# Kernel tuning notes

Hardware: AMD Instinct MI355X
Metric: run time of the kernel (lower is better)

## Reference

```python
import jax, jax.numpy as jnp
import numpy as np

RO = 4.0
STRIDE = 1.0
DILATIONS = (1, 1, 1, 2, 2, 4, 4)  # deep-snake res blocks


def conv2d(x, w, b, pad):
    y = jax.lax.conv_general_dilated(x, w, (1, 1), [(pad, pad), (pad, pad)],
                                     dimension_numbers=('NCHW', 'OIHW', 'NCHW'))
    return y + b[None, :, None, None]


def circ_conv(x, w, b, dilation):
    # x: [N, C, V]; circular (wrap) padding of n_adj*dilation on each side, kernel size 9 (n_adj=4)
    pad = (w.shape[-1] // 2) * dilation
    xp = jnp.concatenate([x[..., -pad:], x, x[..., :pad]], axis=-1)
    y = jax.lax.conv_general_dilated(xp, w, (1,), 'VALID', rhs_dilation=(dilation,),
                                     dimension_numbers=('NCH', 'OIH', 'NCH'))
    return y + b[None, :, None]


def bn(x, gamma, beta):
    # BatchNorm1d in eval mode (running_mean=0, running_var=1)
    return x * gamma[None, :, None] + beta[None, :, None]


def conv1x1(x, w, b):
    return jnp.einsum('oc,ncv->nov', w, x) + b[None, :, None]


def grid_sample_polys(feat, polys, ind):
    # feat: [B, C, H, W]; polys: [N, V, 2] (x, y) in feature-map pixel coords; ind: [N]
    # torch grid_sample(bilinear, align_corners=False, zeros pad) after the deep-snake
    # normalization x/(w/2)-1 reduces to sampling at (px-0.5, py-0.5).
    B, C, H, W = feat.shape
    ix = polys[..., 0] - 0.5
    iy = polys[..., 1] - 0.5
    x0 = jnp.floor(ix)
    y0 = jnp.floor(iy)
    wx = (ix - x0)[..., None]
    wy = (iy - y0)[..., None]
    x0i = x0.astype(jnp.int32)
    y0i = y0.astype(jnp.int32)

    def gather(yi, xi):
        valid = (xi >= 0) & (xi < W) & (yi >= 0) & (yi < H)
        xc = jnp.clip(xi, 0, W - 1)
        yc = jnp.clip(yi, 0, H - 1)
        v = feat[ind[:, None], :, yc, xc]  # [N, V, C]
        return v * valid[..., None]

    v00 = gather(y0i, x0i)
    v01 = gather(y0i, x0i + 1)
    v10 = gather(y0i + 1, x0i)
    v11 = gather(y0i + 1, x0i + 1)
    out = (v00 * (1 - wx) * (1 - wy) + v01 * wx * (1 - wy)
           + v10 * (1 - wx) * wy + v11 * wx * wy)
    return out.transpose(0, 2, 1)  # [N, C, V]


def snake_forward(x, head_w, head_b, head_g, head_bt, res_w, res_b, res_g, res_bt,
                  fus_w, fus_b, pw1, pb1, pw2, pb2, pw3, pb3):
    # Deep-snake Snake with conv_type='dgrid': head + 7 residual dilated circular convs,
    # fusion 1x1 + global max pool, then 3-layer 1x1 prediction head -> 2 offsets.
    h = bn(jax.nn.relu(circ_conv(x, head_w, head_b, 1)), head_g, head_bt)
    states = [h]
    cur = h
    for i, d in enumerate(DILATIONS):
        y = bn(jax.nn.relu(circ_conv(cur, res_w[i], res_b[i], d)), res_g[i], res_bt[i])
        cur = y + cur
        states.append(cur)
    state = jnp.concatenate(states, axis=1)  # [N, 8*state_dim, V]
    g = conv1x1(state, fus_w, fus_b)
    g = jnp.max(g, axis=2, keepdims=True)
    g = jnp.broadcast_to(g, (state.shape[0], g.shape[1], state.shape[2]))
    s = jnp.concatenate([g, state], axis=1)
    h1 = jax.nn.relu(conv1x1(s, pw1, pb1))
    h2 = jax.nn.relu(conv1x1(h1, pw2, pb2))
    return conv1x1(h2, pw3, pb3)  # [N, 2, V]


def setup_inputs() -> dict:
    key = jax.random.key(0)
    ks = jax.random.split(key, 24)
    B, C_IN, H, W = 8, 66, 128, 128
    NP, V = 128, 128
    SD = 128           # Snake state_dim = num_vertex
    FD = 66            # snake feature_dim = c_out_proj + 2
    K = 9              # 2*n_adj + 1
    nres = len(DILATIONS)
    s = 0.01  # torch init: normal_(0, 0.01)
    inp = {
        'cnn_feature': jax.random.normal(ks[0], (B, C_IN, H, W), jnp.float32),
        'i_it_poly': jax.random.uniform(ks[1], (NP, V, 2), jnp.float32) * (W - 1),
        'c_it_poly': jax.random.normal(ks[2], (NP, V, 2), jnp.float32) * 0.25,
        'ind': jax.random.randint(ks[3], (NP,), 0, B, jnp.int32),
        'proj_w1': jax.random.normal(ks[4], (256, C_IN, 3, 3), jnp.float32) * s,
        'proj_b1': jnp.zeros((256,), jnp.float32),
        'proj_w2': jax.random.normal(ks[5], (64, 256, 1, 1), jnp.float32) * s,
        'proj_b2': jnp.zeros((64,), jnp.float32),
        'head_w': jax.random.normal(ks[6], (SD, FD, K), jnp.float32) * s,
        'head_b': jnp.zeros((SD,), jnp.float32),
        'head_g': jnp.ones((SD,), jnp.float32),
        'head_bt': jnp.zeros((SD,), jnp.float32),
        'res_w': jax.random.normal(ks[7], (nres, SD, SD, K), jnp.float32) * s,
        'res_b': jnp.zeros((nres, SD), jnp.float32),
        'res_g': jnp.ones((nres, SD), jnp.float32),
        'res_bt': jnp.zeros((nres, SD), jnp.float32),
        'fus_w': jax.random.normal(ks[8], (256, SD * (nres + 1)), jnp.float32) * s,
        'fus_b': jnp.zeros((256,), jnp.float32),
        'pw1': jax.random.normal(ks[9], (256, SD * (nres + 1) + 256), jnp.float32) * s,
        'pb1': jnp.zeros((256,), jnp.float32),
        'pw2': jax.random.normal(ks[10], (64, 256), jnp.float32) * s,
        'pb2': jnp.zeros((64,), jnp.float32),
        'pw3': jax.random.normal(ks[11], (2, 64), jnp.float32) * s,
        'pb3': jnp.zeros((2,), jnp.float32),
    }
    return inp


def reference(cnn_feature, i_it_poly, c_it_poly, ind,
              proj_w1, proj_b1, proj_w2, proj_b2,
              head_w, head_b, head_g, head_bt,
              res_w, res_b, res_g, res_bt,
              fus_w, fus_b, pw1, pb1, pw2, pb2, pw3, pb3):
    # projection: conv3x3 -> relu -> conv1x1  (66 -> 256 -> 64)
    feat = jax.nn.relu(conv2d(cnn_feature, proj_w1, proj_b1, 1))
    feat = conv2d(feat, proj_w2, proj_b2, 0)
    # gather per-vertex features via bilinear grid sampling (get_gcn_feature)
    vert_feat = grid_sample_polys(feat, i_it_poly, ind)          # [N, 64, V]
    coords = (c_it_poly * RO).transpose(0, 2, 1)                  # [N, 2, V]
    init_input = jnp.concatenate([vert_feat, coords], axis=1)     # [N, 66, V]
    offset = snake_forward(init_input, head_w, head_b, head_g, head_bt,
                           res_w, res_b, res_g, res_bt,
                           fus_w, fus_b, pw1, pb1, pw2, pb2, pw3, pb3)
    i_poly = i_it_poly * RO + offset.transpose(0, 2, 1) * STRIDE  # [N, V, 2]
    return i_poly
```

## Files before the change

### kernel.cpp

```cpp
#include <hip/hip_runtime.h>
#include <hip/hip_bf16.h>

constexpr int B   = 8;
constexpr int CIN = 66;
constexpr int H   = 128, W = 128;
constexpr int C1  = 256;
constexpr int NP  = 128;
constexpr int V   = 128;
constexpr int SD  = 128;
constexpr int NRES = 7;
constexpr float RO = 4.0f;

typedef __bf16 bf16x8 __attribute__((ext_vector_type(8)));
typedef float  f32x4  __attribute__((ext_vector_type(4)));
typedef unsigned short u16x8 __attribute__((ext_vector_type(8)));

__device__ inline float bfu2f(unsigned short u) {
    union { unsigned int i; float f; } c; c.i = ((unsigned)u) << 16; return c.f;
}

__global__ __launch_bounds__(256) void k_pack_x(const float* __restrict__ x,
                                                __hip_bfloat16* __restrict__ xp)
{
    const int bi  = blockIdx.x;
    const int b   = bi / 130;
    const int yp  = bi % 130;
    const int tid = threadIdx.x;
    const int y   = yp - 1;
    const bool interior = (y >= 0 && y < H);

    __shared__ float xs[CIN * W];
    if (interior) {
        for (int i = tid; i < CIN * W; i += 256)
            xs[i] = x[((size_t)b * CIN + (i >> 7)) * (H * W) + y * W + (i & 127)];
    }
    __syncthreads();
    __hip_bfloat16* op = xp + ((size_t)b * 130 + yp) * (130 * 72);
    for (int i = tid; i < 130 * 72; i += 256) {
        int xpx = i / 72, c = i - xpx * 72;
        int xx = xpx - 1;
        float v = 0.f;
        if (interior && xx >= 0 && xx < W && c < CIN) v = xs[c * W + xx];
        op[i] = __float2bfloat16(v);
    }
}

__global__ __launch_bounds__(256) void k_pack_weights(
    const float* __restrict__ w3, const float* __restrict__ hw,
    const float* __restrict__ rw, const float* __restrict__ fw,
    const float* __restrict__ ppw1, const float* __restrict__ ppw2,
    __hip_bfloat16* __restrict__ wp2, __hip_bfloat16* __restrict__ wpk2,
    __hip_bfloat16* __restrict__ fwb, __hip_bfloat16* __restrict__ pw1hb,
    __hip_bfloat16* __restrict__ pw2b)
{
    const int bid = blockIdx.x, tid = threadIdx.x;
    if (bid < 256) {
        int oc = bid;
        for (int t = tid; t < 3 * 232; t += 256) {
            int ky = t / 232, s = t - ky * 232;
            float v = 0.f;
            if (s < 216) {
                int kx = s / 72, ic = s - kx * 72;
                if (ic < CIN) v = w3[((size_t)(oc * CIN + ic) * 3 + ky) * 3 + kx];
            }
            wp2[((size_t)ky * 256 + oc) * 232 + s] = __float2bfloat16(v);
        }
    } else if (bid < 1280) {
        int q = bid - 256, l = q >> 7, oc = q & 127;
        for (int t = tid; t < 9 * 128; t += 256) {
            int k = t >> 7, ic = t & 127;
            float v = 0.f;
            if (l == 0) { if (ic < 66) v = hw[((size_t)oc * 66 + ic) * 9 + k]; }
            else v = rw[((((size_t)(l - 1) * 128 + oc) * 128) + ic) * 9 + k];
            int s = ic >> 3, j = ic & 7;
            int sw = ((s ^ (oc & 7)) << 3) + j;
            wpk2[(((size_t)l * 9 + k) * 128 + oc) * 128 + sw] = __float2bfloat16(v);
        }
    } else if (bid < 1536) {
        int r = bid - 1280;
        for (int c = tid; c < 1024; c += 256)
            fwb[(size_t)r * 1024 + c] = __float2bfloat16(fw[(size_t)r * 1024 + c]);
    } else if (bid < 1792) {
        int r = bid - 1536;
        for (int c = tid; c < 1024; c += 256)
            pw1hb[(size_t)r * 1024 + c] = __float2bfloat16(ppw1[(size_t)r * 1280 + 256 + c]);
    } else {
        int r = bid - 1792;
        for (int c = tid; c < 256; c += 256)
            pw2b[(size_t)r * 256 + c] = __float2bfloat16(ppw2[(size_t)r * 256 + c]);
    }
}

__global__ __launch_bounds__(256, 2) void k_conv3x3_mfma(
    const __hip_bfloat16* __restrict__ xp,
    const __hip_bfloat16* __restrict__ wp,
    const float* __restrict__ bias,
    __hip_bfloat16* __restrict__ out)
{
    constexpr int SB = 232;
    __shared__ __hip_bfloat16 ash[9392];
    __shared__ __hip_bfloat16 bsh[128 * SB];

    const int tid = threadIdx.x;
    const int ln  = tid & 63;
    const int wv  = tid >> 6;
    const int wm  = (wv >> 1) * 64;
    const int wn  = (wv & 1) * 64;
    const int l15 = ln & 15;
    const int lhi = ln >> 4;

    const int by  = blockIdx.x;
    const int b   = by >> 7;
    const int y   = by & 127;
    const int ocb = blockIdx.y * 128;

    if (tid < 32) ash[9360 + tid] = __float2bfloat16(0.f);

    f32x4 acc[4][4] = {};

    for (int ky = 0; ky < 3; ++ky) {
        __syncthreads();
        {
            const char* g = (const char*)(xp + ((size_t)b * 130 + y + ky) * 9360);
            for (int off = wv * 1024; off < 18720; off += 4096) {
                int o = off + ln * 16;
                if (o < 18720)
                    __builtin_amdgcn_global_load_lds(
                        (const __attribute__((address_space(1))) void*)(g + o),
                        (__attribute__((address_space(3))) void*)((char*)ash + off),
                        16, 0, 0);
            }
        }
        {
            const char* g = (const char*)(wp + ((size_t)ky * 256 + ocb) * SB);
            for (int off = wv * 1024; off < 59392; off += 4096) {
                int o = off + ln * 16;
                if (o < 59392)
                    __builtin_amdgcn_global_load_lds(
                        (const __attribute__((address_space(1))) void*)(g + o),
                        (__attribute__((address_space(3))) void*)((char*)bsh + off),
                        16, 0, 0);
            }
        }
        __syncthreads();

#pragma unroll
        for (int ks = 0; ks < 7; ++ks) {
            bf16x8 a[4], bq[4];
#pragma unroll
            for (int m = 0; m < 4; ++m) {
                int pos = wm + m * 16 + l15;
                a[m] = *(const bf16x8*)((const char*)ash + pos * 144 + ks * 64 + lhi * 16);
            }
#pragma unroll
            for (int n = 0; n < 4; ++n) {
                int oc = wn + n * 16 + l15;
                bq[n] = *(const bf16x8*)((const char*)bsh + oc * (SB * 2) + ks * 64 + lhi * 16);
            }
#pragma unroll
            for (int m = 0; m < 4; ++m)
#pragma unroll
                for (int n = 0; n < 4; ++n)
                    acc[m][n] = __builtin_amdgcn_mfma_f32_16x16x32_bf16(
                        a[m], bq[n], acc[m][n], 0, 0, 0);
        }
    }

#pragma unroll
    for (int n = 0; n < 4; ++n) {
        int oc = ocb + wn + n * 16 + l15;
        float bb = bias[oc];
#pragma unroll
        for (int m = 0; m < 4; ++m) {
#pragma unroll
            for (int r = 0; r < 4; ++r) {
                int pos = wm + m * 16 + lhi * 4 + r;
                float v = acc[m][n][r] + bb;
                v = v > 0.f ? v : 0.f;
                out[(((size_t)b * 128 + y) * 128 + pos) * 256 + oc] = __float2bfloat16(v);
            }
        }
    }
}

__global__ __launch_bounds__(256) void k_conv1x1_mfma(
    const __hip_bfloat16* __restrict__ feat1,
    const __hip_bfloat16* __restrict__ w2b,
    const float* __restrict__ b2,
    __hip_bfloat16* __restrict__ feat2)
{
    const int tid = threadIdx.x;
    const int ln  = tid & 63;
    const int wv  = tid >> 6;
    const int wm  = wv * 64;
    const int l15 = ln & 15;
    const int lhi = ln >> 4;
    const int pos0 = blockIdx.x * 256;

    __shared__ __hip_bfloat16 wsh[64 * 136];
    for (int i = tid; i < 1024; i += 256) {
        int row = i >> 4, slot = i & 15;
        *(bf16x8*)&wsh[row * 136 + slot * 8] = *(const bf16x8*)(w2b + row * 256 + slot * 8);
    }
    __syncthreads();

    f32x4 acc[4][4] = {};
#pragma unroll
    for (int kk = 0; kk < 8; ++kk) {
        bf16x8 a[4], bq[4];
#pragma unroll
        for (int m = 0; m < 4; ++m)
            a[m] = *(const bf16x8*)(feat1 + (size_t)(pos0 + wm + m * 16 + l15) * 256 + kk * 32 + lhi * 8);
#pragma unroll
        for (int n = 0; n < 4; ++n)
            bq[n] = *(const bf16x8*)&wsh[(n * 16 + l15) * 136 + kk * 32 + lhi * 8];
#pragma unroll
        for (int m = 0; m < 4; ++m)
#pragma unroll
            for (int n = 0; n < 4; ++n)
                acc[m][n] = __builtin_amdgcn_mfma_f32_16x16x32_bf16(a[m], bq[n], acc[m][n], 0, 0, 0);
    }
#pragma unroll
    for (int n = 0; n < 4; ++n) {
        int og = n * 16 + l15;
        float bb = b2[og];
#pragma unroll
        for (int m = 0; m < 4; ++m)
#pragma unroll
            for (int r = 0; r < 4; ++r) {
                int pos = pos0 + wm + m * 16 + lhi * 4 + r;
                feat2[(size_t)pos * 64 + og] = __float2bfloat16(acc[m][n][r] + bb);
            }
    }
}

__global__ __launch_bounds__(256) void k_sample(
    const __hip_bfloat16* __restrict__ feat2, const float* __restrict__ ipoly,
    const float* __restrict__ cpoly, const int* __restrict__ ind,
    __hip_bfloat16* __restrict__ X0)
{
    const int p = blockIdx.x;
    const int v = threadIdx.x & 127;
    const int half = threadIdx.x >> 7;

    float px = ipoly[(p * V + v) * 2 + 0];
    float py = ipoly[(p * V + v) * 2 + 1];
    float ix = px - 0.5f, iy = py - 0.5f;
    float x0f = floorf(ix), y0f = floorf(iy);
    float wx = ix - x0f, wy = iy - y0f;
    int x0 = (int)x0f, y0 = (int)y0f;

    int   xsv[2] = {x0, x0 + 1}, ysv[2] = {y0, y0 + 1};
    float wxs[2] = {1.f - wx, wx}, wys[2] = {1.f - wy, wy};
    float cw[4]; int cbase[4];
#pragma unroll
    for (int jy = 0; jy < 2; ++jy)
#pragma unroll
        for (int jx = 0; jx < 2; ++jx) {
            int xi = xsv[jx], yi = ysv[jy];
            bool ok = (xi >= 0) && (xi < W) && (yi >= 0) && (yi < H);
            int xc = min(max(xi, 0), W - 1);
            int yc = min(max(yi, 0), H - 1);
            cw[jy * 2 + jx]    = wys[jy] * wxs[jx] * (ok ? 1.f : 0.f);
            cbase[jy * 2 + jx] = yc * W + xc;
        }

    const __hip_bfloat16* fb = feat2 + (size_t)ind[p] * (16384 * 64);
    __hip_bfloat16* xr = X0 + ((size_t)p * V + v) * 128;
#pragma unroll
    for (int ch = 0; ch < 4; ++ch) {
        int chh = half * 4 + ch;
        float s[8];
#pragma unroll
        for (int e = 0; e < 8; ++e) s[e] = 0.f;
#pragma unroll
        for (int j = 0; j < 4; ++j) {
            u16x8 t = *(const u16x8*)(fb + (size_t)cbase[j] * 64 + chh * 8);
#pragma unroll
            for (int e = 0; e < 8; ++e) s[e] += cw[j] * bfu2f(t[e]);
        }
#pragma unroll
        for (int e = 0; e < 8; ++e) xr[chh * 8 + e] = __float2bfloat16(s[e]);
    }
    if (half) {
        xr[64] = __float2bfloat16(cpoly[(p * V + v) * 2 + 0] * RO);
        xr[65] = __float2bfloat16(cpoly[(p * V + v) * 2 + 1] * RO);
        for (int c = 66; c < 128; ++c) xr[c] = __float2bfloat16(0.f);
    }
}

__global__ __launch_bounds__(256) void k_snake_mfma(
    const __hip_bfloat16* __restrict__ xin,
    const __hip_bfloat16* __restrict__ wl,
    const float* __restrict__ bias, const float* __restrict__ gamma,
    const float* __restrict__ beta,
    const __hip_bfloat16* __restrict__ resin,
    __hip_bfloat16* __restrict__ out,
    int dil)
{
    const int tid = threadIdx.x;
    const int ln  = tid & 63;
    const int wv  = tid >> 6;
    const int wm  = (wv >> 1) * 64;
    const int wn  = (wv & 1) * 32;
    const int l15 = ln & 15;
    const int lhi = ln >> 4;
    const int p   = blockIdx.x;
    const int ocb = blockIdx.y * 64;

    __shared__ __hip_bfloat16 xs[128 * 136];
    __shared__ __hip_bfloat16 wsh[2 * 64 * 128];

    {
        const char* g = (const char*)(wl + (size_t)ocb * 128);
        for (int off = tid * 16; off < 16384; off += 4096)
            __builtin_amdgcn_global_load_lds(
                (const __attribute__((address_space(1))) void*)(g + off),
                (__attribute__((address_space(3))) void*)((char*)wsh + off), 16, 0, 0);
    }
    const __hip_bfloat16* xb = xin + (size_t)p * (V * 128);
    for (int i = tid; i < 2048; i += 256) {
        int r = i >> 4, slot = i & 15;
        *(bf16x8*)&xs[r * 136 + slot * 8] = *(const bf16x8*)(xb + r * 128 + slot * 8);
    }
    __syncthreads();

    f32x4 acc[4][2] = {};
#pragma unroll 1
    for (int k = 0; k < 9; ++k) {
        if (k < 8) {
            const char* g = (const char*)(wl + (size_t)(k + 1) * (128 * 128) + (size_t)ocb * 128);
            char* dst = (char*)wsh + ((k + 1) & 1) * 16384;
            for (int off = tid * 16; off < 16384; off += 4096)
                __builtin_amdgcn_global_load_lds(
                    (const __attribute__((address_space(1))) void*)(g + off),
                    (__attribute__((address_space(3))) void*)(dst + off), 16, 0, 0);
        }
        const __hip_bfloat16* wbuf = wsh + (k & 1) * 8192;
        const int ofs = (k - 4) * dil + 256;
#pragma unroll
        for (int kc = 0; kc < 4; ++kc) {
            bf16x8 a[4], bq[2];
#pragma unroll
            for (int m = 0; m < 4; ++m) {
                int row = (wm + m * 16 + l15 + ofs) & 127;
                a[m] = *(const bf16x8*)&xs[row * 136 + kc * 32 + lhi * 8];
            }
#pragma unroll
            for (int n = 0; n < 2; ++n) {
                int row  = wn + n * 16 + l15;
                int slot = (kc * 4 + lhi) ^ (row & 7);
                bq[n] = *(const bf16x8*)&wbuf[row * 128 + slot * 8];
            }
#pragma unroll
            for (int m = 0; m < 4; ++m)
#pragma unroll
                for (int n = 0; n < 2; ++n)
                    acc[m][n] = __builtin_amdgcn_mfma_f32_16x16x32_bf16(a[m], bq[n], acc[m][n], 0, 0, 0);
        }
        __syncthreads();
    }

#pragma unroll
    for (int n = 0; n < 2; ++n) {
        int oc = ocb + wn + n * 16 + l15;
        float bb = bias[oc], gg = gamma[oc], bt = beta[oc];
#pragma unroll
        for (int m = 0; m < 4; ++m)
#pragma unroll
            for (int r = 0; r < 4; ++r) {
                int pos = wm + m * 16 + lhi * 4 + r;
                size_t idx = ((size_t)p * V + pos) * 128 + oc;
                float v = acc[m][n][r] + bb;
                v = v > 0.f ? v : 0.f;
                v = v * gg + bt;
                if (resin) v += __bfloat162float(resin[idx]);
                out[idx] = __float2bfloat16(v);
            }
    }
}

__global__ __launch_bounds__(256) void k_vconv1024(
    const __hip_bfloat16* __restrict__ xin,
    const __hip_bfloat16* __restrict__ wb,
    const float* __restrict__ fbias,
    const float* __restrict__ pbias,
    int relu,
    __hip_bfloat16* __restrict__ out)
{
    const int tid = threadIdx.x;
    const int ln  = tid & 63;
    const int wv  = tid >> 6;
    const int wm  = (wv >> 1) * 64;
    const int wn  = (wv & 1) * 64;
    const int l15 = ln & 15;
    const int lhi = ln >> 4;
    const int p   = blockIdx.x;
    const int ocb = blockIdx.y * 128;

    f32x4 acc[4][4] = {};
    for (int s = 0; s < 8; ++s) {
        const __hip_bfloat16* xa = xin + ((size_t)s * NP + p) * (V * 128);
#pragma unroll
        for (int kc = 0; kc < 4; ++kc) {
            bf16x8 a[4], bq[4];
#pragma unroll
            for (int m = 0; m < 4; ++m)
                a[m] = *(const bf16x8*)(xa + (size_t)(wm + m * 16 + l15) * 128 + kc * 32 + lhi * 8);
#pragma unroll
            for (int n = 0; n < 4; ++n)
                bq[n] = *(const bf16x8*)(wb + (size_t)(ocb + wn + n * 16 + l15) * 1024 + s * 128 + kc * 32 + lhi * 8);
#pragma unroll
            for (int m = 0; m < 4; ++m)
#pragma unroll
                for (int n = 0; n < 4; ++n)
                    acc[m][n] = __builtin_amdgcn_mfma_f32_16x16x32_bf16(a[m], bq[n], acc[m][n], 0, 0, 0);
        }
    }
#pragma unroll
    for (int n = 0; n < 4; ++n) {
        int og = ocb + wn + n * 16 + l15;
        float bb = (fbias ? fbias[og] : 0.f) + (pbias ? pbias[(size_t)p * 256 + og] : 0.f);
#pragma unroll
        for (int m = 0; m < 4; ++m)
#pragma unroll
            for (int r = 0; r < 4; ++r) {
                int pos = wm + m * 16 + lhi * 4 + r;
                float v = acc[m][n][r] + bb;
                if (relu) v = v > 0.f ? v : 0.f;
                out[((size_t)p * V + pos) * 256 + og] = __float2bfloat16(v);
            }
    }
}

__global__ __launch_bounds__(128) void k_h2(
    const __hip_bfloat16* __restrict__ h1,
    const __hip_bfloat16* __restrict__ w2b,
    const float* __restrict__ pb2,
    __hip_bfloat16* __restrict__ h2)
{
    const int tid = threadIdx.x;
    const int ln  = tid & 63;
    const int wv  = tid >> 6;
    const int wm  = wv * 64;
    const int l15 = ln & 15;
    const int lhi = ln >> 4;
    const int p   = blockIdx.x;

    f32x4 acc[4][4] = {};
#pragma unroll
    for (int kk = 0; kk < 8; ++kk) {
        bf16x8 a[4], bq[4];
#pragma unroll
        for (int m = 0; m < 4; ++m)
            a[m] = *(const bf16x8*)(h1 + ((size_t)p * V + wm + m * 16 + l15) * 256 + kk * 32 + lhi * 8);
#pragma unroll
        for (int n = 0; n < 4; ++n)
            bq[n] = *(const bf16x8*)(w2b + (size_t)(n * 16 + l15) * 256 + kk * 32 + lhi * 8);
#pragma unroll
        for (int m = 0; m < 4; ++m)
#pragma unroll
            for (int n = 0; n < 4; ++n)
                acc[m][n] = __builtin_amdgcn_mfma_f32_16x16x32_bf16(a[m], bq[n], acc[m][n], 0, 0, 0);
    }
#pragma unroll
    for (int n = 0; n < 4; ++n) {
        int og = n * 16 + l15;
        float bb = pb2[og];
#pragma unroll
        for (int m = 0; m < 4; ++m)
#pragma unroll
            for (int r = 0; r < 4; ++r) {
                int pos = wm + m * 16 + lhi * 4 + r;
                float v = acc[m][n][r] + bb;
                v = v > 0.f ? v : 0.f;
                h2[((size_t)p * V + pos) * 64 + og] = __float2bfloat16(v);
            }
    }
}

__global__ __launch_bounds__(256) void k_gmaxgc(const __hip_bfloat16* __restrict__ fused,
                                                const float* __restrict__ pw1,
                                                const float* __restrict__ pb1,
                                                float* __restrict__ gc)
{
    int p = blockIdx.x, o = threadIdx.x;
    float m = -3.4e38f;
    for (int v = 0; v < V; ++v)
        m = fmaxf(m, __bfloat162float(fused[((size_t)p * V + v) * 256 + o]));
    __shared__ float gl[256];
    gl[o] = m;
    __syncthreads();
    float a = pb1[o];
    const float* wr = pw1 + (size_t)o * 1280;
    for (int c = 0; c < 256; ++c) a += wr[c] * gl[c];
    gc[(size_t)p * 256 + o] = a;
}

__global__ __launch_bounds__(128) void k_final(const __hip_bfloat16* __restrict__ h2,
                                               const float* __restrict__ pw3,
                                               const float* __restrict__ pb3,
                                               const float* __restrict__ ipoly,
                                               float* __restrict__ outp)
{
    int p = blockIdx.x, v = threadIdx.x;
    __shared__ float w3[128];
    w3[v] = pw3[v];
    __syncthreads();
    float a0 = pb3[0], a1 = pb3[1];
    const u16x8* hp = (const u16x8*)(h2 + ((size_t)p * V + v) * 64);
#pragma unroll
    for (int ch = 0; ch < 8; ++ch) {
        u16x8 t = hp[ch];
#pragma unroll
        for (int e = 0; e < 8; ++e) {
            int c = ch * 8 + e;
            float hv = bfu2f(t[e]);
            a0 += w3[c] * hv;
            a1 += w3[64 + c] * hv;
        }
    }
    int idx = (p * V + v) * 2;
    outp[idx]     = ipoly[idx] * RO + a0;
    outp[idx + 1] = ipoly[idx + 1] * RO + a1;
}

extern "C" void kernel_launch(void* const* d_in, const int* in_sizes, int n_in,
                              void* d_out, int out_size, void* d_ws, size_t ws_size,
                              hipStream_t stream)
{
    const float* cnn   = (const float*)d_in[0];
    const float* ipoly = (const float*)d_in[1];
    const float* cpoly = (const float*)d_in[2];
    const int*   ind   = (const int*)d_in[3];
    const float* pw1c  = (const float*)d_in[4];
    const float* pb1c  = (const float*)d_in[5];
    const float* pw2c  = (const float*)d_in[6];
    const float* pb2c  = (const float*)d_in[7];
    const float* hw    = (const float*)d_in[8];
    const float* hb    = (const float*)d_in[9];
    const float* hg    = (const float*)d_in[10];
    const float* hbt   = (const float*)d_in[11];
    const float* rw    = (const float*)d_in[12];
    const float* rb    = (const float*)d_in[13];
    const float* rg    = (const float*)d_in[14];
    const float* rbt   = (const float*)d_in[15];
    const float* fw    = (const float*)d_in[16];
    const float* fb    = (const float*)d_in[17];
    const float* ppw1  = (const float*)d_in[18];
    const float* ppb1  = (const float*)d_in[19];
    const float* ppw2  = (const float*)d_in[20];
    const float* ppb2  = (const float*)d_in[21];
    const float* ppw3  = (const float*)d_in[22];
    const float* ppb3  = (const float*)d_in[23];
    float* outp = (float*)d_out;

    char* ws = (char*)d_ws;
    __hip_bfloat16* feat1  = (__hip_bfloat16*)(ws);
    __hip_bfloat16* states = (__hip_bfloat16*)(ws);
    __hip_bfloat16* fused  = (__hip_bfloat16*)(ws + 33554432);
    __hip_bfloat16* h1     = (__hip_bfloat16*)(ws + 41943040);
    __hip_bfloat16* h2     = (__hip_bfloat16*)(ws + 50331648);
    float*          gcbuf  = (float*)(ws + 52428800);
    __hip_bfloat16* xp     = (__hip_bfloat16*)(ws + 67108864);
    __hip_bfloat16* feat2  = (__hip_bfloat16*)(ws + 67108864);
    __hip_bfloat16* wp2    = (__hip_bfloat16*)(ws + 86577664);
    __hip_bfloat16* wpk2   = (__hip_bfloat16*)(ws + 86934016);
    __hip_bfloat16* fwb    = (__hip_bfloat16*)(ws + 89293312);
    __hip_bfloat16* pw1hb  = (__hip_bfloat16*)(ws + 89817600);
    __hip_bfloat16* pw2b   = (__hip_bfloat16*)(ws + 90341888);
    __hip_bfloat16* X0     = (__hip_bfloat16*)(ws + 90374656);

    k_pack_x<<<dim3(8 * 130), 256, 0, stream>>>(cnn, xp);
    k_pack_weights<<<dim3(1856), 256, 0, stream>>>(pw1c, hw, rw, fw, ppw1, ppw2,
                                                   wp2, wpk2, fwb, pw1hb, pw2b);

    k_conv3x3_mfma<<<dim3(1024, 2), 256, 0, stream>>>(xp, wp2, pb1c, feat1);
    k_conv1x1_mfma<<<dim3(512), 256, 0, stream>>>(feat1, pw2b, pb2c, feat2);
    k_sample<<<dim3(NP), 256, 0, stream>>>(feat2, ipoly, cpoly, ind, X0);

    k_snake_mfma<<<dim3(NP, 2), 256, 0, stream>>>(X0, wpk2, hb, hg, hbt, nullptr,
                                                  states, 1);
    const int dil[NRES] = {1, 1, 1, 2, 2, 4, 4};
    const size_t SSZ = (size_t)NP * V * 128;
    for (int i = 0; i < NRES; ++i) {
        const __hip_bfloat16* xin = states + (size_t)i * SSZ;
        __hip_bfloat16* yout      = states + (size_t)(i + 1) * SSZ;
        const __hip_bfloat16* wi  = wpk2 + (size_t)(i + 1) * 9 * 128 * 128;
        k_snake_mfma<<<dim3(NP, 2), 256, 0, stream>>>(xin, wi, rb + i * SD, rg + i * SD,
                                                      rbt + i * SD, xin, yout, dil[i]);
    }

    k_vconv1024<<<dim3(NP, 2), 256, 0, stream>>>(states, fwb, fb, nullptr, 0, fused);
    k_gmaxgc<<<dim3(NP), 256, 0, stream>>>(fused, ppw1, ppb1, gcbuf);
    k_vconv1024<<<dim3(NP, 2), 256, 0, stream>>>(states, pw1hb, nullptr, gcbuf, 1, h1);
    k_h2<<<dim3(NP), 128, 0, stream>>>(h1, pw2b, ppb2, h2);
    k_final<<<dim3(NP), 128, 0, stream>>>(h2, ppw3, ppb3, ipoly, outp);
}
```

Measured before the change: 453.1 us.

## Fuse snake layers, fusion conv and prediction head into one per-polygon kernel

Replaces the 8 snake-layer launches, the two 1024-channel vertex convs, the global-max kernel and the two prediction-head kernels with a single kernel. Each block owns one polygon and keeps the layer state ping-ponged in LDS. The fusion and first prediction-layer GEMMs are accumulated in registers layer by layer, so the per-layer states, fused and h1 buffers never travel through global memory. Weights are now read straight from global memory without LDS staging or swizzle, and only 128 blocks run, each with a large register accumulator footprint. That trades launch and global-memory overhead for lower parallelism and possible register spills.

```diff
diff --git a/kernel.cpp b/kernel.cpp
--- a/kernel.cpp
+++ b/kernel.cpp
@@ -18,6 +18,7 @@
 __device__ inline float bfu2f(unsigned short u) {
     union { unsigned int i; float f; } c; c.i = ((unsigned)u) << 16; return c.f;
 }
+__device__ inline float b2f(__hip_bfloat16 b) { return __bfloat162float(b); }
 
 __global__ __launch_bounds__(256) void k_pack_x(const float* __restrict__ x,
                                                 __hip_bfloat16* __restrict__ xp)
@@ -51,7 +52,7 @@
     const float* __restrict__ ppw1, const float* __restrict__ ppw2,
     __hip_bfloat16* __restrict__ wp2, __hip_bfloat16* __restrict__ wpk2,
     __hip_bfloat16* __restrict__ fwb, __hip_bfloat16* __restrict__ pw1hb,
-    __hip_bfloat16* __restrict__ pw2b)
+    __hip_bfloat16* __restrict__ pw2b, __hip_bfloat16* __restrict__ pw1gb)
 {
     const int bid = blockIdx.x, tid = threadIdx.x;
     if (bid < 256) {
@@ -72,9 +73,7 @@
             float v = 0.f;
             if (l == 0) { if (ic < 66) v = hw[((size_t)oc * 66 + ic) * 9 + k]; }
             else v = rw[((((size_t)(l - 1) * 128 + oc) * 128) + ic) * 9 + k];
-            int s = ic >> 3, j = ic & 7;
-            int sw = ((s ^ (oc & 7)) << 3) + j;
-            wpk2[(((size_t)l * 9 + k) * 128 + oc) * 128 + sw] = __float2bfloat16(v);
+            wpk2[(((size_t)l * 9 + k) * 128 + oc) * 128 + ic] = __float2bfloat16(v);
         }
     } else if (bid < 1536) {
         int r = bid - 1280;
@@ -84,10 +83,14 @@
         int r = bid - 1536;
         for (int c = tid; c < 1024; c += 256)
             pw1hb[(size_t)r * 1024 + c] = __float2bfloat16(ppw1[(size_t)r * 1280 + 256 + c]);
-    } else {
+    } else if (bid < 1856) {
         int r = bid - 1792;
         for (int c = tid; c < 256; c += 256)
             pw2b[(size_t)r * 256 + c] = __float2bfloat16(ppw2[(size_t)r * 256 + c]);
+    } else {
+        int o = bid - 1856;
+        for (int c = tid; c < 256; c += 256)
+            pw1gb[(size_t)c * 256 + o] = __float2bfloat16(ppw1[(size_t)o * 1280 + c]);
     }
 }
 
@@ -289,240 +292,222 @@
     }
 }
 
-__global__ __launch_bounds__(256) void k_snake_mfma(
-    const __hip_bfloat16* __restrict__ xin,
-    const __hip_bfloat16* __restrict__ wl,
-    const float* __restrict__ bias, const float* __restrict__ gamma,
-    const float* __restrict__ beta,
-    const __hip_bfloat16* __restrict__ resin,
-    __hip_bfloat16* __restrict__ out,
-    int dil)
-{
+__global__ __launch_bounds__(256, 1) void k_mega(
+    const __hip_bfloat16* __restrict__ X0,
+    const __hip_bfloat16* __restrict__ wsnk,
+    const float* __restrict__ hb, const float* __restrict__ hg, const float* __restrict__ hbt,
+    const float* __restrict__ rb, const float* __restrict__ rg, const float* __restrict__ rbt,
+    const __hip_bfloat16* __restrict__ fwb,
+    const float* __restrict__ fb,
+    const __hip_bfloat16* __restrict__ pw1gb,
+    const float* __restrict__ pb1,
+    const __hip_bfloat16* __restrict__ pw1hb,
+    const __hip_bfloat16* __restrict__ pw2b,
+    const float* __restrict__ pb2,
+    const float* __restrict__ pw3, const float* __restrict__ pb3,
+    const float* __restrict__ ipoly,
+    float* __restrict__ outp)
+{
+    __shared__ __hip_bfloat16 s0[128 * 136];
+    __shared__ __hip_bfloat16 s1[128 * 136];
+    __shared__ __hip_bfloat16 h1L[128 * 264];
+    __shared__ float gred[2048];
+    __shared__ float gl[256];
+    __shared__ float gcv[256];
+
     const int tid = threadIdx.x;
     const int ln  = tid & 63;
     const int wv  = tid >> 6;
-    const int wm  = (wv >> 1) * 64;
-    const int wn  = (wv & 1) * 32;
     const int l15 = ln & 15;
     const int lhi = ln >> 4;
+    const int wmv = (wv >> 1) * 64;
+    const int wns = (wv & 1) * 64;
+    const int wno = (wv & 1) * 128;
     const int p   = blockIdx.x;
-    const int ocb = blockIdx.y * 64;
-
-    __shared__ __hip_bfloat16 xs[128 * 136];
-    __shared__ __hip_bfloat16 wsh[2 * 64 * 128];
 
     {
-        const char* g = (const char*)(wl + (size_t)ocb * 128);
-        for (int off = tid * 16; off < 16384; off += 4096)
-            __builtin_amdgcn_global_load_lds(
-                (const __attribute__((address_space(1))) void*)(g + off),
-                (__attribute__((address_space(3))) void*)((char*)wsh + off), 16, 0, 0);
-    }
-    const __hip_bfloat16* xb = xin + (size_t)p * (V * 128);
-    for (int i = tid; i < 2048; i += 256) {
-        int r = i >> 4, slot = i & 15;
-        *(bf16x8*)&xs[r * 136 + slot * 8] = *(const bf16x8*)(xb + r * 128 + slot * 8);
-    }
-    __syncthreads();
-
-    f32x4 acc[4][2] = {};
+        const __hip_bfloat16* xb = X0 + (size_t)p * (V * 128);
+        for (int i = tid; i < 2048; i += 256) {
+            int r = i >> 4, slot = i & 15;
+            *(bf16x8*)&s0[r * 136 + slot * 8] = *(const bf16x8*)(xb + r * 128 + slot * 8);
+        }
+    }
+    __syncthreads();
+
+    f32x4 facc[4][8] = {};
+    f32x4 hacc[4][8] = {};
+    const int dils[8] = {1, 1, 1, 1, 2, 2, 4, 4};
+
 #pragma unroll 1
-    for (int k = 0; k < 9; ++k) {
-        if (k < 8) {
-            const char* g = (const char*)(wl + (size_t)(k + 1) * (128 * 128) + (size_t)ocb * 128);
-            char* dst = (char*)wsh + ((k + 1) & 1) * 16384;
-            for (int off = tid * 16; off < 16384; off += 4096)
-                __builtin_amdgcn_global_load_lds(
-                    (const __attribute__((address_space(1))) void*)(g + off),
-                    (__attribute__((address_space(3))) void*)(dst + off), 16, 0, 0);
-        }
-        const __hip_bfloat16* wbuf = wsh + (k & 1) * 8192;
-        const int ofs = (k - 4) * dil + 256;
+    for (int l = 0; l < 8; ++l) {
+        __hip_bfloat16* cur  = (l & 1) ? s1 : s0;
+        __hip_bfloat16* pong = (l & 1) ? s0 : s1;
+        const __hip_bfloat16* wl = wsnk + (size_t)l * (9 * 128 * 128);
+        const int dil = dils[l];
+
+        f32x4 sacc[4][4] = {};
+#pragma unroll 1
+        for (int k = 0; k < 9; ++k) {
+            const int ofs = (k - 4) * dil + 128;
+            const __hip_bfloat16* wk = wl + (size_t)k * (128 * 128);
+#pragma unroll
+            for (int kc = 0; kc < 4; ++kc) {
+                bf16x8 a[4], bq[4];
+#pragma unroll
+                for (int m = 0; m < 4; ++m) {
+                    int row = (wmv + m * 16 + l15 + ofs) & 127;
+                    a[m] = *(const bf16x8*)&cur[row * 136 + kc * 32 + lhi * 8];
+                }
+#pragma unroll
+                for (int n = 0; n < 4; ++n)
+                    bq[n] = *(const bf16x8*)(wk + (size_t)(wns + n * 16 + l15) * 128 + kc * 32 + lhi * 8);
+#pragma unroll
+                for (int m = 0; m < 4; ++m)
+#pragma unroll
+                    for (int n = 0; n < 4; ++n)
+                        sacc[m][n] = __builtin_amdgcn_mfma_f32_16x16x32_bf16(a[m], bq[n], sacc[m][n], 0, 0, 0);
+            }
+        }
+
+        const float* bbp = l ? (rb  + (l - 1) * 128) : hb;
+        const float* ggp = l ? (rg  + (l - 1) * 128) : hg;
+        const float* btp = l ? (rbt + (l - 1) * 128) : hbt;
+#pragma unroll
+        for (int n = 0; n < 4; ++n) {
+            int oc = wns + n * 16 + l15;
+            float bb = bbp[oc], gg = ggp[oc], bt = btp[oc];
+#pragma unroll
+            for (int m = 0; m < 4; ++m)
+#pragma unroll
+                for (int r = 0; r < 4; ++r) {
+                    int pos = wmv + m * 16 + lhi * 4 + r;
+                    float v = sacc[m][n][r] + bb;
+                    v = v > 0.f ? v : 0.f;
+                    v = v * gg + bt;
+                    if (l) v += b2f(cur[pos * 136 + oc]);
+                    pong[pos * 136 + oc] = __float2bfloat16(v);
+                }
+        }
+        __syncthreads();
+
 #pragma unroll
         for (int kc = 0; kc < 4; ++kc) {
-            bf16x8 a[4], bq[2];
-#pragma unroll
-            for (int m = 0; m < 4; ++m) {
-                int row = (wm + m * 16 + l15 + ofs) & 127;
-                a[m] = *(const bf16x8*)&xs[row * 136 + kc * 32 + lhi * 8];
-            }
-#pragma unroll
-            for (int n = 0; n < 2; ++n) {
-                int row  = wn + n * 16 + l15;
-                int slot = (kc * 4 + lhi) ^ (row & 7);
-                bq[n] = *(const bf16x8*)&wbuf[row * 128 + slot * 8];
-            }
+            bf16x8 a2[4], bqf[8], bqh[8];
+#pragma unroll
+            for (int m = 0; m < 4; ++m)
+                a2[m] = *(const bf16x8*)&pong[(wmv + m * 16 + l15) * 136 + kc * 32 + lhi * 8];
+#pragma unroll
+            for (int n = 0; n < 8; ++n) {
+                size_t row = (size_t)(wno + n * 16 + l15);
+                bqf[n] = *(const bf16x8*)(fwb   + row * 1024 + l * 128 + kc * 32 + lhi * 8);
+                bqh[n] = *(const bf16x8*)(pw1hb + row * 1024 + l * 128 + kc * 32 + lhi * 8);
+            }
+#pragma unroll
+            for (int m = 0; m < 4; ++m)
+#pragma unroll
+                for (int n = 0; n < 8; ++n) {
+                    facc[m][n] = __builtin_amdgcn_mfma_f32_16x16x32_bf16(a2[m], bqf[n], facc[m][n], 0, 0, 0);
+                    hacc[m][n] = __builtin_amdgcn_mfma_f32_16x16x32_bf16(a2[m], bqh[n], hacc[m][n], 0, 0, 0);
+                }
+        }
+    }
+
+#pragma unroll
+    for (int n = 0; n < 8; ++n) {
+        f32x4 t = facc[0][n];
+        float mm = fmaxf(fmaxf(t[0], t[1]), fmaxf(t[2], t[3]));
+#pragma unroll
+        for (int m = 1; m < 4; ++m) {
+            f32x4 u = facc[m][n];
+            mm = fmaxf(mm, fmaxf(fmaxf(u[0], u[1]), fmaxf(u[2], u[3])));
+        }
+        gred[(wv >> 1) * 1024 + lhi * 256 + wno + n * 16 + l15] = mm;
+    }
+    __syncthreads();
+    {
+        int o = tid;
+        float g = gred[o];
+#pragma unroll
+        for (int q = 1; q < 8; ++q)
+            g = fmaxf(g, gred[(q >> 2) * 1024 + (q & 3) * 256 + o]);
+        gl[o] = g + fb[o];
+    }
+    __syncthreads();
+    {
+        int o = tid;
+        float a = pb1[o];
+        for (int c = 0; c < 256; ++c)
+            a += b2f(pw1gb[(size_t)c * 256 + o]) * gl[c];
+        gcv[o] = a;
+    }
+    __syncthreads();
+
+#pragma unroll
+    for (int n = 0; n < 8; ++n) {
+        int oc = wno + n * 16 + l15;
+        float gco = gcv[oc];
+#pragma unroll
+        for (int m = 0; m < 4; ++m)
+#pragma unroll
+            for (int r = 0; r < 4; ++r) {
+                int v = wmv + m * 16 + lhi * 4 + r;
+                float hv = hacc[m][n][r] + gco;
+                hv = hv > 0.f ? hv : 0.f;
+                h1L[v * 264 + oc] = __float2bfloat16(hv);
+            }
+    }
+    __syncthreads();
+
+    {
+        const int wm2 = (wv >> 1) * 64;
+        const int wn2 = (wv & 1) * 32;
+        f32x4 acc2[4][2] = {};
+#pragma unroll
+        for (int kk = 0; kk < 8; ++kk) {
+            bf16x8 a3[4], bq3[2];
+#pragma unroll
+            for (int m = 0; m < 4; ++m)
+                a3[m] = *(const bf16x8*)&h1L[(wm2 + m * 16 + l15) * 264 + kk * 32 + lhi * 8];
+#pragma unroll
+            for (int n = 0; n < 2; ++n)
+                bq3[n] = *(const bf16x8*)(pw2b + (size_t)(wn2 + n * 16 + l15) * 256 + kk * 32 + lhi * 8);
 #pragma unroll
             for (int m = 0; m < 4; ++m)
 #pragma unroll
                 for (int n = 0; n < 2; ++n)
-                    acc[m][n] = __builtin_amdgcn_mfma_f32_16x16x32_bf16(a[m], bq[n], acc[m][n], 0, 0, 0);
-        }
-        __syncthreads();
-    }
-
-#pragma unroll
-    for (int n = 0; n < 2; ++n) {
-        int oc = ocb + wn + n * 16 + l15;
-        float bb = bias[oc], gg = gamma[oc], bt = beta[oc];
-#pragma unroll
-        for (int m = 0; m < 4; ++m)
-#pragma unroll
-            for (int r = 0; r < 4; ++r) {
-                int pos = wm + m * 16 + lhi * 4 + r;
-                size_t idx = ((size_t)p * V + pos) * 128 + oc;
-                float v = acc[m][n][r] + bb;
-                v = v > 0.f ? v : 0.f;
-                v = v * gg + bt;
-                if (resin) v += __bfloat162float(resin[idx]);
-                out[idx] = __float2bfloat16(v);
-            }
-    }
-}
-
-__global__ __launch_bounds__(256) void k_vconv1024(
-    const __hip_bfloat16* __restrict__ xin,
-    const __hip_bfloat16* __restrict__ wb,
-    const float* __restrict__ fbias,
-    const float* __restrict__ pbias,
-    int relu,
-    __hip_bfloat16* __restrict__ out)
-{
-    const int tid = threadIdx.x;
-    const int ln  = tid & 63;
-    const int wv  = tid >> 6;
-    const int wm  = (wv >> 1) * 64;
-    const int wn  = (wv & 1) * 64;
-    const int l15 = ln & 15;
-    const int lhi = ln >> 4;
-    const int p   = blockIdx.x;
-    const int ocb = blockIdx.y * 128;
-
-    f32x4 acc[4][4] = {};
-    for (int s = 0; s < 8; ++s) {
-        const __hip_bfloat16* xa = xin + ((size_t)s * NP + p) * (V * 128);
-#pragma unroll
-        for (int kc = 0; kc < 4; ++kc) {
-            bf16x8 a[4], bq[4];
-#pragma unroll
-            for (int m = 0; m < 4; ++m)
-                a[m] = *(const bf16x8*)(xa + (size_t)(wm + m * 16 + l15) * 128 + kc * 32 + lhi * 8);
-#pragma unroll
-            for (int n = 0; n < 4; ++n)
-                bq[n] = *(const bf16x8*)(wb + (size_t)(ocb + wn + n * 16 + l15) * 1024 + s * 128 + kc * 32 + lhi * 8);
-#pragma unroll
-            for (int m = 0; m < 4; ++m)
-#pragma unroll
-                for (int n = 0; n < 4; ++n)
-                    acc[m][n] = __builtin_amdgcn_mfma_f32_16x16x32_bf16(a[m], bq[n], acc[m][n], 0, 0, 0);
-        }
-    }
-#pragma unroll
-    for (int n = 0; n < 4; ++n) {
-        int og = ocb + wn + n * 16 + l15;
-        float bb = (fbias ? fbias[og] : 0.f) + (pbias ? pbias[(size_t)p * 256 + og] : 0.f);
-#pragma unroll
-        for (int m = 0; m < 4; ++m)
-#pragma unroll
-            for (int r = 0; r < 4; ++r) {
-                int pos = wm + m * 16 + lhi * 4 + r;
-                float v = acc[m][n][r] + bb;
-                if (relu) v = v > 0.f ? v : 0.f;
-                out[((size_t)p * V + pos) * 256 + og] = __float2bfloat16(v);
-            }
-    }
-}
-
-__global__ __launch_bounds__(128) void k_h2(
-    const __hip_bfloat16* __restrict__ h1,
-    const __hip_bfloat16* __restrict__ w2b,
-    const float* __restrict__ pb2,
-    __hip_bfloat16* __restrict__ h2)
-{
-    const int tid = threadIdx.x;
-    const int ln  = tid & 63;
-    const int wv  = tid >> 6;
-    const int wm  = wv * 64;
-    const int l15 = ln & 15;
-    const int lhi = ln >> 4;
-    const int p   = blockIdx.x;
-
-    f32x4 acc[4][4] = {};
-#pragma unroll
-    for (int kk = 0; kk < 8; ++kk) {
-        bf16x8 a[4], bq[4];
-#pragma unroll
-        for (int m = 0; m < 4; ++m)
-            a[m] = *(const bf16x8*)(h1 + ((size_t)p * V + wm + m * 16 + l15) * 256 + kk * 32 + lhi * 8);
-#pragma unroll
-        for (int n = 0; n < 4; ++n)
-            bq[n] = *(const bf16x8*)(w2b + (size_t)(n * 16 + l15) * 256 + kk * 32 + lhi * 8);
-#pragma unroll
-        for (int m = 0; m < 4; ++m)
-#pragma unroll
-            for (int n = 0; n < 4; ++n)
-                acc[m][n] = __builtin_amdgcn_mfma_f32_16x16x32_bf16(a[m], bq[n], acc[m][n], 0, 0, 0);
-    }
-#pragma unroll
-    for (int n = 0; n < 4; ++n) {
-        int og = n * 16 + l15;
-        float bb = pb2[og];
-#pragma unroll
-        for (int m = 0; m < 4; ++m)
-#pragma unroll
-            for (int r = 0; r < 4; ++r) {
-                int pos = wm + m * 16 + lhi * 4 + r;
-                float v = acc[m][n][r] + bb;
-                v = v > 0.f ? v : 0.f;
-                h2[((size_t)p * V + pos) * 64 + og] = __float2bfloat16(v);
-            }
-    }
-}
-
-__global__ __launch_bounds__(256) void k_gmaxgc(const __hip_bfloat16* __restrict__ fused,
-                                                const float* __restrict__ pw1,
-                                                const float* __restrict__ pb1,
-                                                float* __restrict__ gc)
-{
-    int p = blockIdx.x, o = threadIdx.x;
-    float m = -3.4e38f;
-    for (int v = 0; v < V; ++v)
-        m = fmaxf(m, __bfloat162float(fused[((size_t)p * V + v) * 256 + o]));
-    __shared__ float gl[256];
-    gl[o] = m;
-    __syncthreads();
-    float a = pb1[o];
-    const float* wr = pw1 + (size_t)o * 1280;
-    for (int c = 0; c < 256; ++c) a += wr[c] * gl[c];
-    gc[(size_t)p * 256 + o] = a;
-}
-
-__global__ __launch_bounds__(128) void k_final(const __hip_bfloat16* __restrict__ h2,
-                                               const float* __restrict__ pw3,
-                                               const float* __restrict__ pb3,
-                                               const float* __restrict__ ipoly,
-                                               float* __restrict__ outp)
-{
-    int p = blockIdx.x, v = threadIdx.x;
-    __shared__ float w3[128];
-    w3[v] = pw3[v];
-    __syncthreads();
-    float a0 = pb3[0], a1 = pb3[1];
-    const u16x8* hp = (const u16x8*)(h2 + ((size_t)p * V + v) * 64);
-#pragma unroll
-    for (int ch = 0; ch < 8; ++ch) {
-        u16x8 t = hp[ch];
-#pragma unroll
-        for (int e = 0; e < 8; ++e) {
-            int c = ch * 8 + e;
-            float hv = bfu2f(t[e]);
-            a0 += w3[c] * hv;
-            a1 += w3[64 + c] * hv;
-        }
-    }
-    int idx = (p * V + v) * 2;
-    outp[idx]     = ipoly[idx] * RO + a0;
-    outp[idx + 1] = ipoly[idx + 1] * RO + a1;
+                    acc2[m][n] = __builtin_amdgcn_mfma_f32_16x16x32_bf16(a3[m], bq3[n], acc2[m][n], 0, 0, 0);
+        }
+        __hip_bfloat16* h2L = s0;
+#pragma unroll
+        for (int n = 0; n < 2; ++n) {
+            int oc2 = wn2 + n * 16 + l15;
+            float bb = pb2[oc2];
+#pragma unroll
+            for (int m = 0; m < 4; ++m)
+#pragma unroll
+                for (int r = 0; r < 4; ++r) {
+                    int v = wm2 + m * 16 + lhi * 4 + r;
+                    float hv = acc2[m][n][r] + bb;
+                    hv = hv > 0.f ? hv : 0.f;
+                    h2L[v * 72 + oc2] = __float2bfloat16(hv);
+                }
+        }
+    }
+    __syncthreads();
+
+    if (tid < 128) {
+        int v = tid;
+        const __hip_bfloat16* h2L = s0;
+        float a0 = pb3[0], a1 = pb3[1];
+        for (int c = 0; c < 64; ++c) {
+            float hv = b2f(h2L[v * 72 + c]);
+            a0 += pw3[c] * hv;
+            a1 += pw3[64 + c] * hv;
+        }
+        int idx = (p * V + v) * 2;
+        outp[idx]     = ipoly[idx] * RO + a0;
+        outp[idx + 1] = ipoly[idx + 1] * RO + a1;
+    }
 }
 
 extern "C" void kernel_launch(void* const* d_in, const int* in_sizes, int n_in,
@@ -557,11 +542,6 @@
 
     char* ws = (char*)d_ws;
     __hip_bfloat16* feat1  = (__hip_bfloat16*)(ws);
-    __hip_bfloat16* states = (__hip_bfloat16*)(ws);
-    __hip_bfloat16* fused  = (__hip_bfloat16*)(ws + 33554432);
-    __hip_bfloat16* h1     = (__hip_bfloat16*)(ws + 41943040);
-    __hip_bfloat16* h2     = (__hip_bfloat16*)(ws + 50331648);
-    float*          gcbuf  = (float*)(ws + 52428800);
     __hip_bfloat16* xp     = (__hip_bfloat16*)(ws + 67108864);
     __hip_bfloat16* feat2  = (__hip_bfloat16*)(ws + 67108864);
     __hip_bfloat16* wp2    = (__hip_bfloat16*)(ws + 86577664);
@@ -569,31 +549,17 @@
     __hip_bfloat16* fwb    = (__hip_bfloat16*)(ws + 89293312);
     __hip_bfloat16* pw1hb  = (__hip_bfloat16*)(ws + 89817600);
     __hip_bfloat16* pw2b   = (__hip_bfloat16*)(ws + 90341888);
-    __hip_bfloat16* X0     = (__hip_bfloat16*)(ws + 90374656);
+    __hip_bfloat16* pw1gb  = (__hip_bfloat16*)(ws + 90374656);
+    __hip_bfloat16* X0     = (__hip_bfloat16*)(ws + 90505728);
 
     k_pack_x<<<dim3(8 * 130), 256, 0, stream>>>(cnn, xp);
-    k_pack_weights<<<dim3(1856), 256, 0, stream>>>(pw1c, hw, rw, fw, ppw1, ppw2,
-                                                   wp2, wpk2, fwb, pw1hb, pw2b);
+    k_pack_weights<<<dim3(2112), 256, 0, stream>>>(pw1c, hw, rw, fw, ppw1, ppw2,
+                                                   wp2, wpk2, fwb, pw1hb, pw2b, pw1gb);
 
     k_conv3x3_mfma<<<dim3(1024, 2), 256, 0, stream>>>(xp, wp2, pb1c, feat1);
     k_conv1x1_mfma<<<dim3(512), 256, 0, stream>>>(feat1, pw2b, pb2c, feat2);
     k_sample<<<dim3(NP), 256, 0, stream>>>(feat2, ipoly, cpoly, ind, X0);
-
-    k_snake_mfma<<<dim3(NP, 2), 256, 0, stream>>>(X0, wpk2, hb, hg, hbt, nullptr,
-                                                  states, 1);
-    const int dil[NRES] = {1, 1, 1, 2, 2, 4, 4};
-    const size_t SSZ = (size_t)NP * V * 128;
-    for (int i = 0; i < NRES; ++i) {
-        const __hip_bfloat16* xin = states + (size_t)i * SSZ;
-        __hip_bfloat16* yout      = states + (size_t)(i + 1) * SSZ;
-        const __hip_bfloat16* wi  = wpk2 + (size_t)(i + 1) * 9 * 128 * 128;
-        k_snake_mfma<<<dim3(NP, 2), 256, 0, stream>>>(xin, wi, rb + i * SD, rg + i * SD,
-                                                      rbt + i * SD, xin, yout, dil[i]);
-    }
-
-    k_vconv1024<<<dim3(NP, 2), 256, 0, stream>>>(states, fwb, fb, nullptr, 0, fused);
-    k_gmaxgc<<<dim3(NP), 256, 0, stream>>>(fused, ppw1, ppb1, gcbuf);
-    k_vconv1024<<<dim3(NP, 2), 256, 0, stream>>>(states, pw1hb, nullptr, gcbuf, 1, h1);
-    k_h2<<<dim3(NP), 128, 0, stream>>>(h1, pw2b, ppb2, h2);
-    k_final<<<dim3(NP), 128, 0, stream>>>(h2, ppw3, ppb3, ipoly, outp);
-}
+    k_mega<<<dim3(NP), 256, 0, stream>>>(X0, wpk2, hb, hg, hbt, rb, rg, rbt,
+                                         fwb, fb, pw1gb, ppb1, pw1hb, pw2b, ppb2,
+                                         ppw3, ppb3, ipoly, outp);
+}
```

Measured after the change: 505.3 us. 11.5% more time.

## Retile snake conv by vertex quarters with direct global weight loads

Applied to the files above, without the earlier changes.

The snake circular-conv kernel now splits each polygon into four 32-vertex tiles, and every block computes all 128 output channels. Each block stages only its vertex window plus the dilation halo in shared memory. Weights are read straight from global memory (L2-cached) into registers instead of being double-buffered into LDS through async loads, which removes the per-tap barriers and the weight swizzle. The dilation is made a template parameter. In exchange, every block re-reads the full weight tensor from global memory and each wave issues four global weight loads per MFMA group, with no latency hiding across taps.

```diff
diff --git a/kernel.cpp b/kernel.cpp
--- a/kernel.cpp
+++ b/kernel.cpp
@@ -18,6 +18,7 @@
 __device__ inline float bfu2f(unsigned short u) {
     union { unsigned int i; float f; } c; c.i = ((unsigned)u) << 16; return c.f;
 }
+__device__ inline float b2f(__hip_bfloat16 b) { return __bfloat162float(b); }
 
 __global__ __launch_bounds__(256) void k_pack_x(const float* __restrict__ x,
                                                 __hip_bfloat16* __restrict__ xp)
@@ -72,9 +73,7 @@
             float v = 0.f;
             if (l == 0) { if (ic < 66) v = hw[((size_t)oc * 66 + ic) * 9 + k]; }
             else v = rw[((((size_t)(l - 1) * 128 + oc) * 128) + ic) * 9 + k];
-            int s = ic >> 3, j = ic & 7;
-            int sw = ((s ^ (oc & 7)) << 3) + j;
-            wpk2[(((size_t)l * 9 + k) * 128 + oc) * 128 + sw] = __float2bfloat16(v);
+            wpk2[(((size_t)l * 9 + k) * 128 + oc) * 128 + ic] = __float2bfloat16(v);
         }
     } else if (bid < 1536) {
         int r = bid - 1280;
@@ -289,94 +288,67 @@
     }
 }
 
-__global__ __launch_bounds__(256) void k_snake_mfma(
+template <int DIL>
+__global__ __launch_bounds__(256) void k_snake(
     const __hip_bfloat16* __restrict__ xin,
     const __hip_bfloat16* __restrict__ wl,
     const float* __restrict__ bias, const float* __restrict__ gamma,
     const float* __restrict__ beta,
     const __hip_bfloat16* __restrict__ resin,
-    __hip_bfloat16* __restrict__ out,
-    int dil)
-{
+    __hip_bfloat16* __restrict__ out)
+{
+    constexpr int W2 = 32 + 8 * DIL;
     const int tid = threadIdx.x;
     const int ln  = tid & 63;
     const int wv  = tid >> 6;
-    const int wm  = (wv >> 1) * 64;
-    const int wn  = (wv & 1) * 32;
+    const int wmv = (wv >> 1) * 16;
+    const int wn  = (wv & 1) * 64;
     const int l15 = ln & 15;
     const int lhi = ln >> 4;
     const int p   = blockIdx.x;
-    const int ocb = blockIdx.y * 64;
-
-    __shared__ __hip_bfloat16 xs[128 * 136];
-    __shared__ __hip_bfloat16 wsh[2 * 64 * 128];
-
-    {
-        const char* g = (const char*)(wl + (size_t)ocb * 128);
-        for (int off = tid * 16; off < 16384; off += 4096)
-            __builtin_amdgcn_global_load_lds(
-                (const __attribute__((address_space(1))) void*)(g + off),
-                (__attribute__((address_space(3))) void*)((char*)wsh + off), 16, 0, 0);
-    }
+    const int vq  = blockIdx.y * 32;
+
+    __shared__ __hip_bfloat16 xs[W2 * 136];
     const __hip_bfloat16* xb = xin + (size_t)p * (V * 128);
-    for (int i = tid; i < 2048; i += 256) {
+    for (int i = tid; i < W2 * 16; i += 256) {
         int r = i >> 4, slot = i & 15;
-        *(bf16x8*)&xs[r * 136 + slot * 8] = *(const bf16x8*)(xb + r * 128 + slot * 8);
+        int grow = (vq - 4 * DIL + r) & 127;
+        *(bf16x8*)&xs[r * 136 + slot * 8] = *(const bf16x8*)(xb + (size_t)grow * 128 + slot * 8);
     }
     __syncthreads();
 
-    f32x4 acc[4][2] = {};
+    f32x4 acc[4] = {};
 #pragma unroll 1
     for (int k = 0; k < 9; ++k) {
-        if (k < 8) {
-            const char* g = (const char*)(wl + (size_t)(k + 1) * (128 * 128) + (size_t)ocb * 128);
-            char* dst = (char*)wsh + ((k + 1) & 1) * 16384;
-            for (int off = tid * 16; off < 16384; off += 4096)
-                __builtin_amdgcn_global_load_lds(
-                    (const __attribute__((address_space(1))) void*)(g + off),
-                    (__attribute__((address_space(3))) void*)(dst + off), 16, 0, 0);
-        }
-        const __hip_bfloat16* wbuf = wsh + (k & 1) * 8192;
-        const int ofs = (k - 4) * dil + 256;
+        const __hip_bfloat16* wk = wl + (size_t)k * (128 * 128);
+        const int arow = wmv + l15 + k * DIL;
 #pragma unroll
         for (int kc = 0; kc < 4; ++kc) {
-            bf16x8 a[4], bq[2];
-#pragma unroll
-            for (int m = 0; m < 4; ++m) {
-                int row = (wm + m * 16 + l15 + ofs) & 127;
-                a[m] = *(const bf16x8*)&xs[row * 136 + kc * 32 + lhi * 8];
-            }
-#pragma unroll
-            for (int n = 0; n < 2; ++n) {
-                int row  = wn + n * 16 + l15;
-                int slot = (kc * 4 + lhi) ^ (row & 7);
-                bq[n] = *(const bf16x8*)&wbuf[row * 128 + slot * 8];
-            }
-#pragma unroll
-            for (int m = 0; m < 4; ++m)
-#pragma unroll
-                for (int n = 0; n < 2; ++n)
-                    acc[m][n] = __builtin_amdgcn_mfma_f32_16x16x32_bf16(a[m], bq[n], acc[m][n], 0, 0, 0);
-        }
-        __syncthreads();
-    }
-
-#pragma unroll
-    for (int n = 0; n < 2; ++n) {
-        int oc = ocb + wn + n * 16 + l15;
+            bf16x8 a = *(const bf16x8*)&xs[arow * 136 + kc * 32 + lhi * 8];
+            bf16x8 bq[4];
+#pragma unroll
+            for (int n = 0; n < 4; ++n)
+                bq[n] = *(const bf16x8*)(wk + (size_t)(wn + n * 16 + l15) * 128 + kc * 32 + lhi * 8);
+#pragma unroll
+            for (int n = 0; n < 4; ++n)
+                acc[n] = __builtin_amdgcn_mfma_f32_16x16x32_bf16(a, bq[n], acc[n], 0, 0, 0);
+        }
+    }
+
+#pragma unroll
+    for (int n = 0; n < 4; ++n) {
+        int oc = wn + n * 16 + l15;
         float bb = bias[oc], gg = gamma[oc], bt = beta[oc];
 #pragma unroll
-        for (int m = 0; m < 4; ++m)
-#pragma unroll
-            for (int r = 0; r < 4; ++r) {
-                int pos = wm + m * 16 + lhi * 4 + r;
-                size_t idx = ((size_t)p * V + pos) * 128 + oc;
-                float v = acc[m][n][r] + bb;
-                v = v > 0.f ? v : 0.f;
-                v = v * gg + bt;
-                if (resin) v += __bfloat162float(resin[idx]);
-                out[idx] = __float2bfloat16(v);
-            }
+        for (int r = 0; r < 4; ++r) {
+            int pos = vq + wmv + lhi * 4 + r;
+            size_t idx = ((size_t)p * V + pos) * 128 + oc;
+            float v = acc[n][r] + bb;
+            v = v > 0.f ? v : 0.f;
+            v = v * gg + bt;
+            if (resin) v += b2f(resin[idx]);
+            out[idx] = __float2bfloat16(v);
+        }
     }
 }
 
@@ -487,7 +459,7 @@
     int p = blockIdx.x, o = threadIdx.x;
     float m = -3.4e38f;
     for (int v = 0; v < V; ++v)
-        m = fmaxf(m, __bfloat162float(fused[((size_t)p * V + v) * 256 + o]));
+        m = fmaxf(m, b2f(fused[((size_t)p * V + v) * 256 + o]));
     __shared__ float gl[256];
     gl[o] = m;
     __syncthreads();
@@ -579,16 +551,22 @@
     k_conv1x1_mfma<<<dim3(512), 256, 0, stream>>>(feat1, pw2b, pb2c, feat2);
     k_sample<<<dim3(NP), 256, 0, stream>>>(feat2, ipoly, cpoly, ind, X0);
 
-    k_snake_mfma<<<dim3(NP, 2), 256, 0, stream>>>(X0, wpk2, hb, hg, hbt, nullptr,
-                                                  states, 1);
+    k_snake<1><<<dim3(NP, 4), 256, 0, stream>>>(X0, wpk2, hb, hg, hbt, nullptr, states);
     const int dil[NRES] = {1, 1, 1, 2, 2, 4, 4};
     const size_t SSZ = (size_t)NP * V * 128;
     for (int i = 0; i < NRES; ++i) {
         const __hip_bfloat16* xin = states + (size_t)i * SSZ;
         __hip_bfloat16* yout      = states + (size_t)(i + 1) * SSZ;
         const __hip_bfloat16* wi  = wpk2 + (size_t)(i + 1) * 9 * 128 * 128;
-        k_snake_mfma<<<dim3(NP, 2), 256, 0, stream>>>(xin, wi, rb + i * SD, rg + i * SD,
-                                                      rbt + i * SD, xin, yout, dil[i]);
+        if (dil[i] == 1)
+            k_snake<1><<<dim3(NP, 4), 256, 0, stream>>>(xin, wi, rb + i * SD, rg + i * SD,
+                                                        rbt + i * SD, xin, yout);
+        else if (dil[i] == 2)
+            k_snake<2><<<dim3(NP, 4), 256, 0, stream>>>(xin, wi, rb + i * SD, rg + i * SD,
+                                                        rbt + i * SD, xin, yout);
+        else
+            k_snake<4><<<dim3(NP, 4), 256, 0, stream>>>(xin, wi, rb + i * SD, rg + i * SD,
+                                                        rbt + i * SD, xin, yout);
     }
 
     k_vconv1024<<<dim3(NP, 2), 256, 0, stream>>>(states, fwb, fb, nullptr, 0, fused);
```

After: 623.1 us. +37.5%, slower.
